# Kernel tuning notes

Measured on AMD Instinct MI355X. Metric: run time of the kernel, lower is better.

The kernel has to match this reference:

```python
import jax, jax.numpy as jnp
import numpy as np

ALPHA = 1.0  # initial_alpha; forward uses self.alpha which stays at init value

def setup_inputs() -> dict:
    key = jax.random.key(0)
    k1, k2, k3, k4 = jax.random.split(key, 4)
    B, T, N, C, K = 8, 32, 2048, 64, 32
    R_seq = jax.random.normal(k1, (B, T, N, C), dtype=jnp.float32)
    W = jax.random.normal(k2, (K, C), dtype=jnp.float32) * (1.0 / np.sqrt(C))
    b = jax.random.normal(k3, (K,), dtype=jnp.float32) * 0.01
    cent = jax.random.normal(k4, (K, C), dtype=jnp.float32)
    centroids = cent / jnp.linalg.norm(cent, axis=1, keepdims=True)  # xavier + L2-normalize rows
    return {"R_seq": R_seq, "W": W, "b": b, "centroids": centroids}

def reference(R_seq, W, b, centroids):
    B, T, N, C = R_seq.shape
    K = centroids.shape[0]
    r = R_seq.reshape(B * T, N, C)                       # (BT, N, C)
    logits = (jnp.einsum('mnc,kc->mnk', r, W) + b) * ALPHA
    a = jax.nn.softmax(logits, axis=-1)                  # (BT, N, K)
    # NetVLAD algebraic decomposition: v_k = a_k^T r - (sum_n a_nk) * c_k
    v = jnp.einsum('mnk,mnc->mkc', a, r) - a.sum(axis=1)[:, :, None] * centroids[None]
    return v.reshape(B, T, K, C)
```

## Files before the change

### kernel.cpp

```cpp
#include <hip/hip_runtime.h>
#include <stdint.h>

typedef __attribute__((ext_vector_type(8))) short bf16x8;
typedef __attribute__((ext_vector_type(4))) short bf16x4;
typedef __attribute__((ext_vector_type(4))) float f32x4;

#define WAVES 8
#define R_STRIDE 72
#define A_STRIDE 40
#define R_LDS_SHORTS (32 * R_STRIDE)
#define A_LDS_SHORTS (32 * A_STRIDE)
#define WAVE_LDS (R_LDS_SHORTS + A_LDS_SHORTS)
#define VB_STRIDE 68

static __device__ __forceinline__ unsigned short f2bf(float f) {
    union { float f; unsigned int i; } x; x.f = f;
    unsigned int i = x.i;
    return (unsigned short)((i + 0x7FFFu + ((i >> 16) & 1u)) >> 16);
}

static __device__ __forceinline__ bf16x8 cvt8(float4 a, float4 b) {
    bf16x8 r;
    r[0] = (short)f2bf(a.x); r[1] = (short)f2bf(a.y);
    r[2] = (short)f2bf(a.z); r[3] = (short)f2bf(a.w);
    r[4] = (short)f2bf(b.x); r[5] = (short)f2bf(b.y);
    r[6] = (short)f2bf(b.z); r[7] = (short)f2bf(b.w);
    return r;
}

static __device__ __forceinline__ float row_sum16(float x) {
    union fi { float f; int i; };
    fi a, b; a.f = x;
    b.i = __builtin_amdgcn_mov_dpp(a.i, 0x128, 0xf, 0xf, false); a.f += b.f;
    b.i = __builtin_amdgcn_mov_dpp(a.i, 0x124, 0xf, 0xf, false); a.f += b.f;
    b.i = __builtin_amdgcn_mov_dpp(a.i, 0x122, 0xf, 0xf, false); a.f += b.f;
    b.i = __builtin_amdgcn_mov_dpp(a.i, 0x121, 0xf, 0xf, false); a.f += b.f;
    return a.f;
}


__global__ __launch_bounds__(512, 2)
void netvlad_fused(const float* __restrict__ R,
                   const float* __restrict__ W,
                   const float* __restrict__ bias,
                   const float* __restrict__ cent,
                   float* __restrict__ out)
{
    __shared__ short smem[WAVES * WAVE_LDS];
    __shared__ float suma_buf[4][32];

    const int tid  = threadIdx.x;
    const int wave = tid >> 6;
    const int lane = tid & 63;
    const int l15  = lane & 15;
    const int quad = lane >> 4;
    const int m    = blockIdx.x;

    short* r_lds = smem + wave * WAVE_LDS;
    short* a_lds = r_lds + R_LDS_SHORTS;

    const float* Rm = R + (size_t)m * (2048 * 64);

    bf16x8 wf[2][2];
#pragma unroll
    for (int kt = 0; kt < 2; ++kt)
#pragma unroll
        for (int cc = 0; cc < 2; ++cc) {
            const float* wp = W + (kt*16 + l15)*64 + cc*32 + quad*8;
            wf[kt][cc] = cvt8(*(const float4*)wp, *(const float4*)(wp + 4));
        }

    float bval[2];
    bval[0] = bias[l15];
    bval[1] = bias[16 + l15];

    f32x4 acc[2][4];
#pragma unroll
    for (int kt = 0; kt < 2; ++kt)
#pragma unroll
        for (int ct = 0; ct < 4; ++ct)
            acc[kt][ct] = (f32x4){0.f, 0.f, 0.f, 0.f};
    float suma[2] = {0.f, 0.f};

    float4 cur[2][2][2];
#pragma unroll
    for (int s = 0; s < 2; ++s)
#pragma unroll
        for (int cc = 0; cc < 2; ++cc) {
            const float* rp = Rm + (size_t)(wave*32 + s*16 + l15)*64 + cc*32 + quad*8;
            cur[s][cc][0] = *(const float4*)rp;
            cur[s][cc][1] = *(const float4*)(rp + 4);
        }

#pragma unroll
    for (int it = 0; it < 8; ++it) {
        float4 nxt[2][2][2];
        if (it < 7) {
            const int n0n = ((it+1)*WAVES + wave) * 32;
#pragma unroll
            for (int s = 0; s < 2; ++s)
#pragma unroll
                for (int cc = 0; cc < 2; ++cc) {
                    const float* rp = Rm + (size_t)(n0n + s*16 + l15)*64 + cc*32 + quad*8;
                    nxt[s][cc][0] = *(const float4*)rp;
                    nxt[s][cc][1] = *(const float4*)(rp + 4);
                }
        }

        bf16x8 af[2][2];
#pragma unroll
        for (int s = 0; s < 2; ++s) {
            const int g = (s*2 + (l15 >> 3)) & 3;
#pragma unroll
            for (int cc = 0; cc < 2; ++cc) {
                af[s][cc] = cvt8(cur[s][cc][0], cur[s][cc][1]);
                const int c0s = (cc*32 + quad*8) ^ (g << 4);
                *(bf16x8*)(r_lds + (s*16 + l15)*R_STRIDE + c0s) = af[s][cc];
            }
        }

        f32x4 d1[2][2];
#pragma unroll
        for (int s = 0; s < 2; ++s)
#pragma unroll
            for (int kt = 0; kt < 2; ++kt) {
                f32x4 d = (f32x4){0.f, 0.f, 0.f, 0.f};
                d = __builtin_amdgcn_mfma_f32_16x16x32_bf16(af[s][0], wf[kt][0], d, 0, 0, 0);
                d = __builtin_amdgcn_mfma_f32_16x16x32_bf16(af[s][1], wf[kt][1], d, 0, 0, 0);
                d1[s][kt] = d;
            }

#pragma unroll
        for (int s = 0; s < 2; ++s) {
            bf16x4 p0, p1;
            float a0s = 0.f, a1s = 0.f;
#pragma unroll
            for (int r = 0; r < 4; ++r) {
                float l0 = d1[s][0][r] + bval[0];
                float l1 = d1[s][1][r] + bval[1];
                float e0 = __expf(l0);
                float e1 = __expf(l1);
                float ss = row_sum16(e0 + e1);
                float rs = __builtin_amdgcn_rcpf(ss);
                float a0 = e0 * rs, a1 = e1 * rs;
                a0s += a0; a1s += a1;
                p0[r] = (short)f2bf(a0);
                p1[r] = (short)f2bf(a1);
            }
            suma[0] += a0s; suma[1] += a1s;
            *(bf16x4*)(a_lds + l15*A_STRIDE        + s*16 + quad*4) = p0;
            *(bf16x4*)(a_lds + (16 + l15)*A_STRIDE + s*16 + quad*4) = p1;
        }

        bf16x8 a2[2];
#pragma unroll
        for (int kt = 0; kt < 2; ++kt)
            a2[kt] = *(bf16x8*)(a_lds + (kt*16 + l15)*A_STRIDE + quad*8);

#pragma unroll
        for (int ct = 0; ct < 4; ++ct) {
            const short* bp = r_lds + (quad*8)*R_STRIDE + ((ct ^ quad) << 4) + l15;
            bf16x8 b2;
#pragma unroll
            for (int j = 0; j < 8; ++j)
                b2[j] = bp[j*R_STRIDE];
#pragma unroll
            for (int kt = 0; kt < 2; ++kt)
                acc[kt][ct] = __builtin_amdgcn_mfma_f32_16x16x32_bf16(a2[kt], b2, acc[kt][ct], 0, 0, 0);
        }

        if (it < 7) {
#pragma unroll
            for (int s = 0; s < 2; ++s)
#pragma unroll
                for (int cc = 0; cc < 2; ++cc) {
                    cur[s][cc][0] = nxt[s][cc][0];
                    cur[s][cc][1] = nxt[s][cc][1];
                }
        }
    }

#pragma unroll
    for (int kt = 0; kt < 2; ++kt) {
        suma[kt] += __shfl_xor(suma[kt], 16);
        suma[kt] += __shfl_xor(suma[kt], 32);
    }

    float* vbuf = (float*)smem;
    __syncthreads();
#pragma unroll
    for (int step = 4; step >= 1; step >>= 1) {
        if (wave >= step && wave < 2*step) {
            float* dst = vbuf + (wave - step) * (32 * VB_STRIDE);
#pragma unroll
            for (int kt = 0; kt < 2; ++kt)
#pragma unroll
                for (int ct = 0; ct < 4; ++ct)
#pragma unroll
                    for (int r = 0; r < 4; ++r)
                        dst[(kt*16 + quad*4 + r)*VB_STRIDE + ct*16 + l15] = acc[kt][ct][r];
            if (lane < 16) {
                suma_buf[wave - step][lane]      = suma[0];
                suma_buf[wave - step][lane + 16] = suma[1];
            }
        }
        __syncthreads();
        if (wave < step) {
            const float* src = vbuf + wave * (32 * VB_STRIDE);
#pragma unroll
            for (int kt = 0; kt < 2; ++kt)
#pragma unroll
                for (int ct = 0; ct < 4; ++ct)
#pragma unroll
                    for (int r = 0; r < 4; ++r)
                        acc[kt][ct][r] += src[(kt*16 + quad*4 + r)*VB_STRIDE + ct*16 + l15];
            suma[0] += suma_buf[wave][l15];
            suma[1] += suma_buf[wave][l15 + 16];
        }
        __syncthreads();
    }

    if (wave == 0) {
        float* op = out + (size_t)m * (32*64);
#pragma unroll
        for (int kt = 0; kt < 2; ++kt) {
#pragma unroll
            for (int r = 0; r < 4; ++r) {
                const int k = kt*16 + quad*4 + r;
                const float su = __shfl(suma[kt], quad*4 + r);
#pragma unroll
                for (int ct = 0; ct < 4; ++ct) {
                    const int c = ct*16 + l15;
                    const float cv = cent[k*64 + c];
                    op[k*64 + c] = acc[kt][ct][r] - su * cv;
                }
            }
        }
    }
}

extern "C" void kernel_launch(void* const* d_in, const int* in_sizes, int n_in,
                              void* d_out, int out_size, void* d_ws, size_t ws_size,
                              hipStream_t stream) {
    (void)in_sizes; (void)n_in; (void)out_size; (void)d_ws; (void)ws_size;
    const float* R = (const float*)d_in[0];
    const float* W = (const float*)d_in[1];
    const float* b = (const float*)d_in[2];
    const float* c = (const float*)d_in[3];
    float* out = (float*)d_out;

    hipLaunchKernelGGL(netvlad_fused, dim3(256), dim3(512), 0, stream, R, W, b, c, out);
}
```

Baseline: 203.1 us.

## Split each NetVLAD item across two blocks with a separate combine kernel

Each (b,t) item's 2048 rows are now split across two blocks, giving 512 blocks instead of 256 so the grid fills more CUs. Partial sums and soft-assignment totals go to a workspace, and a second small kernel adds the halves and subtracts the centroid term. The explicit register double-buffer prefetch of R is dropped and launch bounds are raised to 4 blocks per CU. The cost is a second launch, workspace traffic, and relying on the compiler and occupancy to hide load latency.

```diff
diff --git a/kernel.cpp b/kernel.cpp
--- a/kernel.cpp
+++ b/kernel.cpp
@@ -12,6 +12,8 @@
 #define A_LDS_SHORTS (32 * A_STRIDE)
 #define WAVE_LDS (R_LDS_SHORTS + A_LDS_SHORTS)
 #define VB_STRIDE 68
+#define NITER 4
+#define WS_STRIDE 2080
 
 static __device__ __forceinline__ unsigned short f2bf(float f) {
     union { float f; unsigned int i; } x; x.f = f;
@@ -39,12 +41,11 @@
 }
 
 
-__global__ __launch_bounds__(512, 2)
-void netvlad_fused(const float* __restrict__ R,
-                   const float* __restrict__ W,
-                   const float* __restrict__ bias,
-                   const float* __restrict__ cent,
-                   float* __restrict__ out)
+__global__ __launch_bounds__(512, 4)
+void netvlad_partial(const float* __restrict__ R,
+                     const float* __restrict__ W,
+                     const float* __restrict__ bias,
+                     float* __restrict__ ws)
 {
     __shared__ short smem[WAVES * WAVE_LDS];
     __shared__ float suma_buf[4][32];
@@ -54,12 +55,14 @@
     const int lane = tid & 63;
     const int l15  = lane & 15;
     const int quad = lane >> 4;
-    const int m    = blockIdx.x;
+    const int bid  = blockIdx.x;
+    const int m    = bid >> 1;
+    const int h    = bid & 1;
 
     short* r_lds = smem + wave * WAVE_LDS;
     short* a_lds = r_lds + R_LDS_SHORTS;
 
-    const float* Rm = R + (size_t)m * (2048 * 64);
+    const float* Rm = R + ((size_t)m * 2048 + (size_t)h * 1024) * 64;
 
     bf16x8 wf[2][2];
 #pragma unroll
@@ -82,30 +85,19 @@
             acc[kt][ct] = (f32x4){0.f, 0.f, 0.f, 0.f};
     float suma[2] = {0.f, 0.f};
 
-    float4 cur[2][2][2];
-#pragma unroll
-    for (int s = 0; s < 2; ++s)
-#pragma unroll
-        for (int cc = 0; cc < 2; ++cc) {
-            const float* rp = Rm + (size_t)(wave*32 + s*16 + l15)*64 + cc*32 + quad*8;
-            cur[s][cc][0] = *(const float4*)rp;
-            cur[s][cc][1] = *(const float4*)(rp + 4);
-        }
-
-#pragma unroll
-    for (int it = 0; it < 8; ++it) {
-        float4 nxt[2][2][2];
-        if (it < 7) {
-            const int n0n = ((it+1)*WAVES + wave) * 32;
-#pragma unroll
-            for (int s = 0; s < 2; ++s)
-#pragma unroll
-                for (int cc = 0; cc < 2; ++cc) {
-                    const float* rp = Rm + (size_t)(n0n + s*16 + l15)*64 + cc*32 + quad*8;
-                    nxt[s][cc][0] = *(const float4*)rp;
-                    nxt[s][cc][1] = *(const float4*)(rp + 4);
-                }
-        }
+#pragma unroll
+    for (int it = 0; it < NITER; ++it) {
+        const int n0 = it * (WAVES * 32) + wave * 32;
+
+        float4 cur[2][2][2];
+#pragma unroll
+        for (int s = 0; s < 2; ++s)
+#pragma unroll
+            for (int cc = 0; cc < 2; ++cc) {
+                const float* rp = Rm + (size_t)(n0 + s*16 + l15)*64 + cc*32 + quad*8;
+                cur[s][cc][0] = *(const float4*)rp;
+                cur[s][cc][1] = *(const float4*)(rp + 4);
+            }
 
         bf16x8 af[2][2];
 #pragma unroll
@@ -168,16 +160,6 @@
             for (int kt = 0; kt < 2; ++kt)
                 acc[kt][ct] = __builtin_amdgcn_mfma_f32_16x16x32_bf16(a2[kt], b2, acc[kt][ct], 0, 0, 0);
         }
-
-        if (it < 7) {
-#pragma unroll
-            for (int s = 0; s < 2; ++s)
-#pragma unroll
-                for (int cc = 0; cc < 2; ++cc) {
-                    cur[s][cc][0] = nxt[s][cc][0];
-                    cur[s][cc][1] = nxt[s][cc][1];
-                }
-        }
     }
 
 #pragma unroll
@@ -221,33 +203,60 @@
     }
 
     if (wave == 0) {
-        float* op = out + (size_t)m * (32*64);
-#pragma unroll
-        for (int kt = 0; kt < 2; ++kt) {
+        float* wp = ws + (size_t)bid * WS_STRIDE;
+#pragma unroll
+        for (int kt = 0; kt < 2; ++kt)
 #pragma unroll
             for (int r = 0; r < 4; ++r) {
                 const int k = kt*16 + quad*4 + r;
-                const float su = __shfl(suma[kt], quad*4 + r);
-#pragma unroll
-                for (int ct = 0; ct < 4; ++ct) {
-                    const int c = ct*16 + l15;
-                    const float cv = cent[k*64 + c];
-                    op[k*64 + c] = acc[kt][ct][r] - su * cv;
-                }
-            }
-        }
-    }
+#pragma unroll
+                for (int ct = 0; ct < 4; ++ct)
+                    wp[k*64 + ct*16 + l15] = acc[kt][ct][r];
+            }
+        if (lane < 16) {
+            wp[2048 + lane]      = suma[0];
+            wp[2048 + 16 + lane] = suma[1];
+        }
+    }
+}
+
+__global__ __launch_bounds__(512)
+void netvlad_combine(const float* __restrict__ ws,
+                     const float* __restrict__ cent,
+                     float* __restrict__ out)
+{
+    const int m   = blockIdx.x;
+    const int tid = threadIdx.x;
+    const float* p0 = ws + (size_t)(2*m) * WS_STRIDE;
+    const float* p1 = p0 + WS_STRIDE;
+
+    const int k  = tid >> 4;
+    const int c0 = (tid & 15) << 2;
+    const float s = p0[2048 + k] + p1[2048 + k];
+
+    const int off = k*64 + c0;
+    const float4 v0 = *(const float4*)(p0 + off);
+    const float4 v1 = *(const float4*)(p1 + off);
+    const float4 cv = *(const float4*)(cent + off);
+    float4 o;
+    o.x = v0.x + v1.x - s * cv.x;
+    o.y = v0.y + v1.y - s * cv.y;
+    o.z = v0.z + v1.z - s * cv.z;
+    o.w = v0.w + v1.w - s * cv.w;
+    *(float4*)(out + (size_t)m * 2048 + off) = o;
 }
 
 extern "C" void kernel_launch(void* const* d_in, const int* in_sizes, int n_in,
                               void* d_out, int out_size, void* d_ws, size_t ws_size,
                               hipStream_t stream) {
-    (void)in_sizes; (void)n_in; (void)out_size; (void)d_ws; (void)ws_size;
+    (void)in_sizes; (void)n_in; (void)out_size; (void)ws_size;
     const float* R = (const float*)d_in[0];
     const float* W = (const float*)d_in[1];
     const float* b = (const float*)d_in[2];
     const float* c = (const float*)d_in[3];
     float* out = (float*)d_out;
-
-    hipLaunchKernelGGL(netvlad_fused, dim3(256), dim3(512), 0, stream, R, W, b, c, out);
-}
+    float* ws  = (float*)d_ws;
+
+    hipLaunchKernelGGL(netvlad_partial, dim3(512), dim3(512), 0, stream, R, W, b, ws);
+    hipLaunchKernelGGL(netvlad_combine, dim3(256), dim3(512), 0, stream, ws, c, out);
+}
```

Result: slower. 226.2 us (+11.4%).
